# Performance work log

Measured on AMD Instinct MI355X. Metric: run time of the kernel, lower is better.

The kernel has to match this reference:

```python
import jax, jax.numpy as jnp
import numpy as np

B, T, E, C, I_E, O = 4, 2048, 8, 512, 512, 4096


def setup_inputs() -> dict:
    key = jax.random.key(0)
    k1, k2, k3, k4 = jax.random.split(key, 4)
    x = jax.random.normal(k1, (B, E, C, I_E), dtype=jnp.float32)
    combine_array = jax.random.uniform(k2, (B, T, E, C), dtype=jnp.float32)
    W = jax.random.normal(k3, (E, O, I_E), dtype=jnp.float32) * (1.0 / np.sqrt(I_E))
    b = jax.random.normal(k4, (O,), dtype=jnp.float32) * 0.02
    return {"x": x, "combine_array": combine_array, "W": W, "b": b}


def reference(x, combine_array, W, b):
    # per-expert grouped GEMM: [B,E,C,I_e] x [E,O,I_e] -> [B,E,C,O]
    expert_outputs = jnp.einsum('beci,eoi->beco', x, W) + b
    # expert-choice combine: [B,E,C,O] x [B,T,E,C] -> [B,T,O]
    combined = jnp.einsum('beco,btec->bto', expert_outputs, combine_array)
    return combined
```

## Files before the change

kernel.cpp:

```cpp
#include <hip/hip_runtime.h>
#include <hip/hip_bf16.h>
#include <cstdint>

constexpr int NB = 4;
constexpr int NT = 2048;
constexpr int NE = 8;
constexpr int NC = 512;
constexpr int NI = 512;
constexpr int NO = 4096;
constexpr int NEC = NE * NC;

typedef __attribute__((ext_vector_type(8))) short short8;
typedef __attribute__((ext_vector_type(8))) unsigned short ushort8;
typedef __attribute__((ext_vector_type(4))) float f32x4;

__device__ __forceinline__ unsigned short f2bf(float f) {
  unsigned int u = __builtin_bit_cast(unsigned int, f);
  u += 0x7FFFu + ((u >> 16) & 1u);
  return (unsigned short)(u >> 16);
}

__device__ __forceinline__ ushort8 cvt8(float4 a, float4 b) {
  ushort8 v;
  v[0] = f2bf(a.x); v[1] = f2bf(a.y); v[2] = f2bf(a.z); v[3] = f2bf(a.w);
  v[4] = f2bf(b.x); v[5] = f2bf(b.y); v[6] = f2bf(b.z); v[7] = f2bf(b.w);
  return v;
}

__device__ __forceinline__ int lds_byte(int row, int kbyte) {
  return (row * 64 + kbyte) ^ ((row & 6) << 3);
}

__device__ __forceinline__ void gload_lds16(const void* g, void* lds) {
  __builtin_amdgcn_global_load_lds(
      (const __attribute__((address_space(1))) unsigned int*)g,
      (__attribute__((address_space(3))) unsigned int*)lds, 16, 0, 0);
}

__global__ __launch_bounds__(256) void k_cvt(
    const float* __restrict__ src, unsigned short* __restrict__ dst, int n8) {
  int i = blockIdx.x * blockDim.x + threadIdx.x;
  const int stride = gridDim.x * blockDim.x;
  for (; i < n8; i += stride) {
    const float4* s = (const float4*)(src + (size_t)i * 8);
    float4 a = s[0], b = s[1];
    *(ushort8*)(dst + (size_t)i * 8) = cvt8(a, b);
  }
}

template <int NKT>
__device__ __forceinline__ void gemm8_core(
    const unsigned short* __restrict__ Ag,
    const unsigned short* __restrict__ Bg,
    const int ldk, unsigned short* lds, f32x4 (&acc)[8][4]) {
  const int tid = threadIdx.x, lane = tid & 63, wv = tid >> 6;
  const int wr = wv >> 2, wc = wv & 3;
  const int g16 = lane >> 4;
  const int fr  = lane & 15;
  const int pc  = (g16 ^ ((fr >> 1) & 3)) << 4;

  const int scg = (lane & 3) ^ ((lane >> 3) & 3);
  const size_t srow0 = (size_t)(wv * 16 + (lane >> 2)) * ldk + scg * 8;
  const size_t srowstep = (size_t)128 * ldk;
  const int sdst0 = wv * 512;

#define ASLOT(D, KH) ((D) * 16384 + (KH) * 8192)
#define BSLOT(D, KH) (32768 + (D) * 16384 + (KH) * 8192)
#define STG(PTR, SLOT, KT, KH)                                                \
  {                                                                           \
    const unsigned short* _g = (PTR) + srow0 + (size_t)(KT) * 64 + (KH) * 32; \
    gload_lds16(_g, lds + (SLOT) + sdst0);                                    \
    gload_lds16(_g + srowstep, lds + (SLOT) + 4096 + sdst0);                  \
  }
#define RD8(SLOT, R) \
  (*(const short8*)((const char*)lds + (SLOT) * 2 + (R) * 64 + pc))

  short8 afA[4], afB[4], bfA[4], bfB[4];

#define LDA4(SET, D, KH, MH)                                        \
  _Pragma("unroll") for (int m = 0; m < 4; ++m) {                   \
    SET[m] = RD8(ASLOT(D, KH), wr * 128 + (MH) * 64 + m * 16 + fr); \
  }
#define LDB4(SET, D, KH)                                            \
  _Pragma("unroll") for (int n = 0; n < 4; ++n) {                   \
    SET[n] = RD8(BSLOT(D, KH), wc * 64 + n * 16 + fr);              \
  }
#define MFMAQ(ASET, BSET, MH)                                        \
  __builtin_amdgcn_s_setprio(1);                                     \
  _Pragma("unroll") for (int m = 0; m < 4; ++m)                      \
  _Pragma("unroll") for (int n = 0; n < 4; ++n) {                    \
    acc[(MH) * 4 + m][n] = __builtin_amdgcn_mfma_f32_16x16x32_bf16(  \
        ASET[m], BSET[n], acc[(MH) * 4 + m][n], 0, 0, 0);            \
  }                                                                  \
  __builtin_amdgcn_s_setprio(0);
#define LG4()                                          \
  asm volatile("s_waitcnt lgkmcnt(4)" ::: "memory");   \
  __builtin_amdgcn_sched_barrier(0)
#define LG8()                                          \
  asm volatile("s_waitcnt lgkmcnt(8)" ::: "memory");   \
  __builtin_amdgcn_sched_barrier(0)
#define VM6() asm volatile("s_waitcnt vmcnt(6)" ::: "memory")
#define BAR() __builtin_amdgcn_s_barrier()

  STG(Ag, ASLOT(0, 0), 0, 0); STG(Bg, BSLOT(0, 0), 0, 0);
  STG(Ag, ASLOT(0, 1), 0, 1); STG(Bg, BSLOT(0, 1), 0, 1);
  STG(Ag, ASLOT(1, 0), 1, 0); STG(Bg, BSLOT(1, 0), 1, 0);
  asm volatile("s_waitcnt vmcnt(8)" ::: "memory");
  BAR();
  LDA4(afA, 0, 0, 0); LDB4(bfA, 0, 0);

  for (int it = 0; it < NKT / 2; ++it) {
    const int k1 = (2 * it + 1) & (NKT - 1);
    const int k2 = (2 * it + 2) & (NKT - 1);
    const int k3 = (2 * it + 3) & (NKT - 1);
    STG(Ag, ASLOT(1, 1), k1, 1);
    VM6();
    LDA4(afB, 0, 0, 1);
    LG4();
    MFMAQ(afA, bfA, 0);
    BAR();
    STG(Bg, BSLOT(1, 1), k1, 1);
    LDA4(afA, 0, 1, 0); LDB4(bfB, 0, 1);
    LG8();
    MFMAQ(afB, bfA, 1);
    BAR();
    STG(Ag, ASLOT(0, 0), k2, 0);
    VM6();
    LDA4(afB, 0, 1, 1);
    LG4();
    MFMAQ(afA, bfB, 0);
    BAR();
    STG(Bg, BSLOT(0, 0), k2, 0);
    LDA4(afA, 1, 0, 0); LDB4(bfA, 1, 0);
    LG8();
    MFMAQ(afB, bfB, 1);
    BAR();
    STG(Ag, ASLOT(0, 1), k2, 1);
    VM6();
    LDA4(afB, 1, 0, 1);
    LG4();
    MFMAQ(afA, bfA, 0);
    BAR();
    STG(Bg, BSLOT(0, 1), k2, 1);
    LDA4(afA, 1, 1, 0); LDB4(bfB, 1, 1);
    LG8();
    MFMAQ(afB, bfA, 1);
    BAR();
    STG(Ag, ASLOT(1, 0), k3, 0);
    VM6();
    LDA4(afB, 1, 1, 1);
    LG4();
    MFMAQ(afA, bfB, 0);
    BAR();
    STG(Bg, BSLOT(1, 0), k3, 0);
    LDA4(afA, 0, 0, 0); LDB4(bfA, 0, 0);
    LG8();
    MFMAQ(afB, bfB, 1);
    BAR();
  }
  asm volatile("s_waitcnt vmcnt(0) lgkmcnt(0)" ::: "memory");
#undef ASLOT
#undef BSLOT
#undef STG
#undef RD8
#undef LDA4
#undef LDB4
#undef MFMAQ
#undef LG4
#undef LG8
#undef VM6
#undef BAR
}

__global__ __launch_bounds__(512, 2) void k_gemm1p(
    const unsigned short* __restrict__ Wb, const unsigned short* __restrict__ xb,
    const float* __restrict__ bias, unsigned short* __restrict__ eoT) {
  const int bid = (blockIdx.x & 7) * 128 + (blockIdx.x >> 3);
  const int be = bid >> 5, tile = bid & 31;
  const int b = be >> 3, e = be & 7;
  const int bm = tile >> 1, bn = tile & 1;

  const int tid = threadIdx.x, lane = tid & 63, wv = tid >> 6;
  const int wr = wv >> 2, wc = wv & 3;
  const int g16 = lane >> 4, fr = lane & 15;

  const unsigned short* Ag = Wb + (size_t)e * NO * NI + (size_t)(bm * 256) * NI;
  const unsigned short* Bg = xb + ((size_t)b * NE + e) * NC * NI + (size_t)(bn * 256) * NI;

  __shared__ __align__(16) unsigned short lds[65536];

  f32x4 acc[8][4];
#pragma unroll
  for (int m = 0; m < 8; ++m)
#pragma unroll
    for (int n = 0; n < 4; ++n) acc[m][n] = (f32x4)0.f;

  gemm8_core<NI / 64>(Ag, Bg, NI, lds, acc);

  const int o0 = bm * 256 + wr * 128;
  const int c0 = bn * 256 + wc * 64;
#pragma unroll
  for (int i = 0; i < 8; ++i) {
#pragma unroll
    for (int j = 0; j < 4; ++j) {
      const int o = o0 + (i >> 2) * 64 + (i & 3) * 16 + g16 * 4 + j;
      const float bv = bias[o];
      const size_t base = (((size_t)b * NO + o) * NE + e) * NC + c0;
#pragma unroll
      for (int n = 0; n < 4; ++n)
        eoT[base + n * 16 + fr] = f2bf(acc[i][n][j] + bv);
    }
  }
}

__global__ __launch_bounds__(512, 2) void k_gemm2p(
    const unsigned short* __restrict__ cb, const unsigned short* __restrict__ eoT,
    float* __restrict__ out) {
  const int bid = (blockIdx.x & 7) * 64 + (blockIdx.x >> 3);
  const int b  = bid >> 7;
  const int bm = (bid >> 4) & 7;
  const int bn = bid & 15;

  const int tid = threadIdx.x, lane = tid & 63, wv = tid >> 6;
  const int wr = wv >> 2, wc = wv & 3;
  const int g16 = lane >> 4, fr = lane & 15;

  const unsigned short* Ag = cb  + (size_t)b * NT * NEC + (size_t)(bm * 256) * NEC;
  const unsigned short* Bg = eoT + (size_t)b * NO * NEC + (size_t)(bn * 256) * NEC;

  __shared__ __align__(16) unsigned short lds[65536];

  f32x4 acc[8][4];
#pragma unroll
  for (int m = 0; m < 8; ++m)
#pragma unroll
    for (int n = 0; n < 4; ++n) acc[m][n] = (f32x4)0.f;

  gemm8_core<NEC / 64>(Ag, Bg, NEC, lds, acc);

  const int t0 = bm * 256 + wr * 128;
  const int o0 = bn * 256 + wc * 64;
#pragma unroll
  for (int i = 0; i < 8; ++i) {
#pragma unroll
    for (int j = 0; j < 4; ++j) {
      const int t = t0 + (i >> 2) * 64 + (i & 3) * 16 + g16 * 4 + j;
      float* op = out + ((size_t)b * NT + t) * NO + o0;
#pragma unroll
      for (int n = 0; n < 4; ++n) op[n * 16 + fr] = acc[i][n][j];
    }
  }
}

__global__ __launch_bounds__(256, 2) void k_gemm1(
    const float* __restrict__ x, const float* __restrict__ W,
    const float* __restrict__ bias, unsigned short* __restrict__ eoT) {
  const int tile = blockIdx.x;
  const int e = blockIdx.y, b = blockIdx.z;
  const int bm = tile >> 2, bn = tile & 3;
  const int tid = threadIdx.x, lane = tid & 63, wv = tid >> 6;
  const int wr = wv >> 1, wc = wv & 1;

  const float* Ag = W + (size_t)e * NO * NI + (size_t)(bm * 128) * NI;
  const float* Bg = x + ((size_t)b * NE + e) * NC * NI + (size_t)(bn * 128) * NI;

  __shared__ __align__(16) unsigned short As[128 * 32];
  __shared__ __align__(16) unsigned short Bs[128 * 32];

  f32x4 acc[4][4];
#pragma unroll
  for (int m = 0; m < 4; ++m)
#pragma unroll
    for (int n = 0; n < 4; ++n) acc[m][n] = (f32x4)0.f;

  for (int k0 = 0; k0 < NI; k0 += 32) {
    __syncthreads();
#pragma unroll
    for (int s = 0; s < 2; ++s) {
      const int q = tid + s * 256;
      const int row = q >> 2, kc = (q & 3) * 8;
      const float* ga = Ag + (size_t)row * NI + k0 + kc;
      float4 a0 = *(const float4*)ga;
      float4 a1 = *(const float4*)(ga + 4);
      *(ushort8*)((char*)As + lds_byte(row, kc * 2)) = cvt8(a0, a1);
      const float* gb = Bg + (size_t)row * NI + k0 + kc;
      float4 b0 = *(const float4*)gb;
      float4 b1 = *(const float4*)(gb + 4);
      *(ushort8*)((char*)Bs + lds_byte(row, kc * 2)) = cvt8(b0, b1);
    }
    __syncthreads();

    const int kb = (lane >> 4) * 16;
    short8 af[4], bfv[4];
#pragma unroll
    for (int m = 0; m < 4; ++m) {
      const int r = wr * 64 + m * 16 + (lane & 15);
      af[m] = *(const short8*)((const char*)As + lds_byte(r, kb));
    }
#pragma unroll
    for (int n = 0; n < 4; ++n) {
      const int r = wc * 64 + n * 16 + (lane & 15);
      bfv[n] = *(const short8*)((const char*)Bs + lds_byte(r, kb));
    }
#pragma unroll
    for (int m = 0; m < 4; ++m)
#pragma unroll
      for (int n = 0; n < 4; ++n)
        acc[m][n] = __builtin_amdgcn_mfma_f32_16x16x32_bf16(
            af[m], bfv[n], acc[m][n], 0, 0, 0);
  }

  const int o0 = bm * 128 + wr * 64;
  const int c0 = bn * 128 + wc * 64;
#pragma unroll
  for (int m = 0; m < 4; ++m) {
#pragma unroll
    for (int j = 0; j < 4; ++j) {
      const int o = o0 + m * 16 + (lane >> 4) * 4 + j;
      const float bv = bias[o];
      const size_t base = (((size_t)b * NO + o) * NE + e) * NC + c0;
#pragma unroll
      for (int n = 0; n < 4; ++n)
        eoT[base + n * 16 + (lane & 15)] = f2bf(acc[m][n][j] + bv);
    }
  }
}

__global__ __launch_bounds__(256, 2) void k_gemm2(
    const float* __restrict__ comb, const unsigned short* __restrict__ eoT,
    float* __restrict__ out) {
  const int b = blockIdx.y;
  const int bm = blockIdx.x >> 5;
  const int bn = blockIdx.x & 31;
  const int tid = threadIdx.x, lane = tid & 63, wv = tid >> 6;
  const int wr = wv >> 1, wc = wv & 1;

  const float* Ag = comb + (size_t)b * NT * NEC + (size_t)(bm * 128) * NEC;
  const unsigned short* Bg = eoT + (size_t)b * NO * NEC + (size_t)(bn * 128) * NEC;

  __shared__ __align__(16) unsigned short As[128 * 32];
  __shared__ __align__(16) unsigned short Bs[128 * 32];

  f32x4 acc[4][4];
#pragma unroll
  for (int m = 0; m < 4; ++m)
#pragma unroll
    for (int n = 0; n < 4; ++n) acc[m][n] = (f32x4)0.f;

  for (int k0 = 0; k0 < NEC; k0 += 32) {
    __syncthreads();
#pragma unroll
    for (int s = 0; s < 2; ++s) {
      const int q = tid + s * 256;
      const int row = q >> 2, kc = (q & 3) * 8;
      const float* ga = Ag + (size_t)row * NEC + k0 + kc;
      float4 a0 = *(const float4*)ga;
      float4 a1 = *(const float4*)(ga + 4);
      *(ushort8*)((char*)As + lds_byte(row, kc * 2)) = cvt8(a0, a1);
      ushort8 bv = *(const ushort8*)(Bg + (size_t)row * NEC + k0 + kc);
      *(ushort8*)((char*)Bs + lds_byte(row, kc * 2)) = bv;
    }
    __syncthreads();

    const int kb = (lane >> 4) * 16;
    short8 af[4], bfv[4];
#pragma unroll
    for (int m = 0; m < 4; ++m) {
      const int r = wr * 64 + m * 16 + (lane & 15);
      af[m] = *(const short8*)((const char*)As + lds_byte(r, kb));
    }
#pragma unroll
    for (int n = 0; n < 4; ++n) {
      const int r = wc * 64 + n * 16 + (lane & 15);
      bfv[n] = *(const short8*)((const char*)Bs + lds_byte(r, kb));
    }
#pragma unroll
    for (int m = 0; m < 4; ++m)
#pragma unroll
      for (int n = 0; n < 4; ++n)
        acc[m][n] = __builtin_amdgcn_mfma_f32_16x16x32_bf16(
            af[m], bfv[n], acc[m][n], 0, 0, 0);
  }

  const int t0 = bm * 128 + wr * 64;
  const int o0 = bn * 128 + wc * 64;
#pragma unroll
  for (int m = 0; m < 4; ++m) {
#pragma unroll
    for (int j = 0; j < 4; ++j) {
      const int t = t0 + m * 16 + (lane >> 4) * 4 + j;
      float* op = out + ((size_t)b * NT + t) * NO + o0;
#pragma unroll
      for (int n = 0; n < 4; ++n) op[n * 16 + (lane & 15)] = acc[m][n][j];
    }
  }
}

extern "C" void kernel_launch(void* const* d_in, const int* in_sizes, int n_in,
                              void* d_out, int out_size, void* d_ws, size_t ws_size,
                              hipStream_t stream) {
  const float* x    = (const float*)d_in[0];
  const float* comb = (const float*)d_in[1];
  const float* W    = (const float*)d_in[2];
  const float* bias = (const float*)d_in[3];
  float* out = (float*)d_out;

  const size_t EOT_ELEMS = (size_t)NB * NO * NE * NC;
  const size_t X_ELEMS   = (size_t)NB * NE * NC * NI;
  const size_t W_ELEMS   = (size_t)NE * NO * NI;
  const size_t C_ELEMS   = (size_t)NB * NT * NE * NC;
  const size_t region2_elems = (C_ELEMS > X_ELEMS + W_ELEMS) ? C_ELEMS : (X_ELEMS + W_ELEMS);
  const size_t need = (EOT_ELEMS + region2_elems) * 2;

  unsigned short* eoT = (unsigned short*)d_ws;

  if (ws_size >= need) {
    unsigned short* reg2 = eoT + EOT_ELEMS;
    unsigned short* xb = reg2;
    unsigned short* Wb = reg2 + X_ELEMS;
    unsigned short* cbp = reg2;

    k_cvt<<<2048, 256, 0, stream>>>(x, xb, (int)(X_ELEMS / 8));
    k_cvt<<<2048, 256, 0, stream>>>(W, Wb, (int)(W_ELEMS / 8));
    k_gemm1p<<<1024, 512, 0, stream>>>(Wb, xb, bias, eoT);
    k_cvt<<<2048, 256, 0, stream>>>(comb, cbp, (int)(C_ELEMS / 8));
    k_gemm2p<<<512, 512, 0, stream>>>(cbp, eoT, out);
  } else {
    k_gemm1<<<dim3(128, NE, NB), 256, 0, stream>>>(x, W, bias, eoT);
    k_gemm2<<<dim3(512, NB), 256, 0, stream>>>(comb, eoT, out);
  }
}
```

Before: 396.6 us.

## Reassociate MoE combine: contract combine weights with x before expert projection

Reorders the two contractions so the combine array is first multiplied with the expert inputs per expert (producing a [B,T,E,I] intermediate), followed by one GEMM against transposed expert weights over E*I. The bias is applied afterward as bias times the per-token sum of combine weights, computed during combine conversion. This lowers the first GEMM's work and halves the intermediate size, but adds transposing conversions for x and W and rounds a different intermediate to bf16.

New measurement: 354.4 us. -10.6%, faster.

```diff
diff --git a/kernel.cpp b/kernel.cpp
--- a/kernel.cpp
+++ b/kernel.cpp
@@ -9,6 +9,7 @@
 constexpr int NI = 512;
 constexpr int NO = 4096;
 constexpr int NEC = NE * NC;
+constexpr int NEI = NE * NI;
 
 typedef __attribute__((ext_vector_type(8))) short short8;
 typedef __attribute__((ext_vector_type(8))) unsigned short ushort8;
@@ -37,14 +38,65 @@
       (__attribute__((address_space(3))) unsigned int*)lds, 16, 0, 0);
 }
 
-__global__ __launch_bounds__(256) void k_cvt(
-    const float* __restrict__ src, unsigned short* __restrict__ dst, int n8) {
-  int i = blockIdx.x * blockDim.x + threadIdx.x;
-  const int stride = gridDim.x * blockDim.x;
-  for (; i < n8; i += stride) {
-    const float4* s = (const float4*)(src + (size_t)i * 8);
-    float4 a = s[0], b = s[1];
-    *(ushort8*)(dst + (size_t)i * 8) = cvt8(a, b);
+
+__global__ __launch_bounds__(256) void k_cvt_comb(
+    const float* __restrict__ comb, unsigned short* __restrict__ cbp,
+    float* __restrict__ S) {
+  const int row = blockIdx.x;
+  const float* src = comb + (size_t)row * NEC;
+  unsigned short* dst = cbp + (size_t)row * NEC;
+  const int tid = threadIdx.x;
+  float sum = 0.f;
+#pragma unroll
+  for (int it = 0; it < 2; ++it) {
+    const int i8 = tid + it * 256;
+    const float4* s = (const float4*)(src + i8 * 8);
+    float4 a = s[0], b4 = s[1];
+    *(ushort8*)(dst + i8 * 8) = cvt8(a, b4);
+    sum += a.x + a.y + a.z + a.w + b4.x + b4.y + b4.z + b4.w;
+  }
+  for (int off = 32; off > 0; off >>= 1) sum += __shfl_down(sum, off);
+  __shared__ float ws4[4];
+  if ((tid & 63) == 0) ws4[tid >> 6] = sum;
+  __syncthreads();
+  if (tid == 0) S[row] = ws4[0] + ws4[1] + ws4[2] + ws4[3];
+}
+
+__global__ __launch_bounds__(256) void k_cvtT_x(
+    const float* __restrict__ x, unsigned short* __restrict__ xT) {
+  const int be = blockIdx.x >> 6;
+  const int tile = blockIdx.x & 63;
+  const int c0 = (tile >> 3) * 64, i0 = (tile & 7) * 64;
+  const float* src = x + (size_t)be * NC * NI;
+  unsigned short* dst = xT + (size_t)be * NI * NC;
+  __shared__ unsigned short tl[64][65];
+  const int lr = threadIdx.x >> 6, lc = threadIdx.x & 63;
+#pragma unroll
+  for (int s = 0; s < 16; ++s) {
+    const int c = s * 4 + lr;
+    tl[c][lc] = f2bf(src[(size_t)(c0 + c) * NI + i0 + lc]);
+  }
+  __syncthreads();
+#pragma unroll
+  for (int s = 0; s < 16; ++s) {
+    const int i = s * 4 + lr;
+    dst[(size_t)(i0 + i) * NC + c0 + lc] = tl[lc][i];
+  }
+}
+
+__global__ __launch_bounds__(256) void k_cvtT_W(
+    const float* __restrict__ W, unsigned short* __restrict__ Wt) {
+  const size_t n8 = (size_t)NE * NO * NI / 8;
+  size_t idx = (size_t)blockIdx.x * 256 + threadIdx.x;
+  const size_t stride = (size_t)gridDim.x * 256;
+  for (; idx < n8; idx += stride) {
+    const int i8 = (int)(idx & (NI / 8 - 1));
+    const size_t eo = idx >> 6;
+    const int e = (int)(eo >> 12);
+    const int o = (int)(eo & 4095);
+    const float4* s = (const float4*)(W + eo * NI + i8 * 8);
+    float4 a = s[0], b4 = s[1];
+    *(ushort8*)(Wt + ((size_t)o * NE + e) * NI + i8 * 8) = cvt8(a, b4);
   }
 }
 
@@ -52,7 +104,7 @@
 __device__ __forceinline__ void gemm8_core(
     const unsigned short* __restrict__ Ag,
     const unsigned short* __restrict__ Bg,
-    const int ldk, unsigned short* lds, f32x4 (&acc)[8][4]) {
+    const int ldkA, const int ldkB, unsigned short* lds, f32x4 (&acc)[8][4]) {
   const int tid = threadIdx.x, lane = tid & 63, wv = tid >> 6;
   const int wr = wv >> 2, wc = wv & 3;
   const int g16 = lane >> 4;
@@ -60,17 +112,19 @@
   const int pc  = (g16 ^ ((fr >> 1) & 3)) << 4;
 
   const int scg = (lane & 3) ^ ((lane >> 3) & 3);
-  const size_t srow0 = (size_t)(wv * 16 + (lane >> 2)) * ldk + scg * 8;
-  const size_t srowstep = (size_t)128 * ldk;
+  const size_t srow0A = (size_t)(wv * 16 + (lane >> 2)) * ldkA + scg * 8;
+  const size_t srow0B = (size_t)(wv * 16 + (lane >> 2)) * ldkB + scg * 8;
+  const size_t srstA = (size_t)128 * ldkA;
+  const size_t srstB = (size_t)128 * ldkB;
   const int sdst0 = wv * 512;
 
 #define ASLOT(D, KH) ((D) * 16384 + (KH) * 8192)
 #define BSLOT(D, KH) (32768 + (D) * 16384 + (KH) * 8192)
-#define STG(PTR, SLOT, KT, KH)                                                \
-  {                                                                           \
-    const unsigned short* _g = (PTR) + srow0 + (size_t)(KT) * 64 + (KH) * 32; \
-    gload_lds16(_g, lds + (SLOT) + sdst0);                                    \
-    gload_lds16(_g + srowstep, lds + (SLOT) + 4096 + sdst0);                  \
+#define STG(PTR, SR0, SRST, SLOT, KT, KH)                                  \
+  {                                                                        \
+    const unsigned short* _g = (PTR) + (SR0) + (size_t)(KT) * 64 + (KH) * 32; \
+    gload_lds16(_g, lds + (SLOT) + sdst0);                                 \
+    gload_lds16(_g + (SRST), lds + (SLOT) + 4096 + sdst0);                 \
   }
 #define RD8(SLOT, R) \
   (*(const short8*)((const char*)lds + (SLOT) * 2 + (R) * 64 + pc))
@@ -102,9 +156,12 @@
 #define VM6() asm volatile("s_waitcnt vmcnt(6)" ::: "memory")
 #define BAR() __builtin_amdgcn_s_barrier()
 
-  STG(Ag, ASLOT(0, 0), 0, 0); STG(Bg, BSLOT(0, 0), 0, 0);
-  STG(Ag, ASLOT(0, 1), 0, 1); STG(Bg, BSLOT(0, 1), 0, 1);
-  STG(Ag, ASLOT(1, 0), 1, 0); STG(Bg, BSLOT(1, 0), 1, 0);
+  STG(Ag, srow0A, srstA, ASLOT(0, 0), 0, 0);
+  STG(Bg, srow0B, srstB, BSLOT(0, 0), 0, 0);
+  STG(Ag, srow0A, srstA, ASLOT(0, 1), 0, 1);
+  STG(Bg, srow0B, srstB, BSLOT(0, 1), 0, 1);
+  STG(Ag, srow0A, srstA, ASLOT(1, 0), 1, 0);
+  STG(Bg, srow0B, srstB, BSLOT(1, 0), 1, 0);
   asm volatile("s_waitcnt vmcnt(8)" ::: "memory");
   BAR();
   LDA4(afA, 0, 0, 0); LDB4(bfA, 0, 0);
@@ -113,46 +170,46 @@
     const int k1 = (2 * it + 1) & (NKT - 1);
     const int k2 = (2 * it + 2) & (NKT - 1);
     const int k3 = (2 * it + 3) & (NKT - 1);
-    STG(Ag, ASLOT(1, 1), k1, 1);
+    STG(Ag, srow0A, srstA, ASLOT(1, 1), k1, 1);
     VM6();
     LDA4(afB, 0, 0, 1);
     LG4();
     MFMAQ(afA, bfA, 0);
     BAR();
-    STG(Bg, BSLOT(1, 1), k1, 1);
+    STG(Bg, srow0B, srstB, BSLOT(1, 1), k1, 1);
     LDA4(afA, 0, 1, 0); LDB4(bfB, 0, 1);
     LG8();
     MFMAQ(afB, bfA, 1);
     BAR();
-    STG(Ag, ASLOT(0, 0), k2, 0);
+    STG(Ag, srow0A, srstA, ASLOT(0, 0), k2, 0);
     VM6();
     LDA4(afB, 0, 1, 1);
     LG4();
     MFMAQ(afA, bfB, 0);
     BAR();
-    STG(Bg, BSLOT(0, 0), k2, 0);
+    STG(Bg, srow0B, srstB, BSLOT(0, 0), k2, 0);
     LDA4(afA, 1, 0, 0); LDB4(bfA, 1, 0);
     LG8();
     MFMAQ(afB, bfB, 1);
     BAR();
-    STG(Ag, ASLOT(0, 1), k2, 1);
+    STG(Ag, srow0A, srstA, ASLOT(0, 1), k2, 1);
     VM6();
     LDA4(afB, 1, 0, 1);
     LG4();
     MFMAQ(afA, bfA, 0);
     BAR();
-    STG(Bg, BSLOT(0, 1), k2, 1);
+    STG(Bg, srow0B, srstB, BSLOT(0, 1), k2, 1);
     LDA4(afA, 1, 1, 0); LDB4(bfB, 1, 1);
     LG8();
     MFMAQ(afB, bfA, 1);
     BAR();
-    STG(Ag, ASLOT(1, 0), k3, 0);
+    STG(Ag, srow0A, srstA, ASLOT(1, 0), k3, 0);
     VM6();
     LDA4(afB, 1, 1, 1);
     LG4();
     MFMAQ(afA, bfB, 0);
     BAR();
-    STG(Bg, BSLOT(1, 0), k3, 0);
+    STG(Bg, srow0B, srstB, BSLOT(1, 0), k3, 0);
     LDA4(afA, 0, 0, 0); LDB4(bfA, 0, 0);
     LG8();
     MFMAQ(afB, bfB, 1);
@@ -172,11 +229,11 @@
 #undef BAR
 }
 
-__global__ __launch_bounds__(512, 2) void k_gemm1p(
-    const unsigned short* __restrict__ Wb, const unsigned short* __restrict__ xb,
-    const float* __restrict__ bias, unsigned short* __restrict__ eoT) {
-  const int bid = (blockIdx.x & 7) * 128 + (blockIdx.x >> 3);
-  const int be = bid >> 5, tile = bid & 31;
+__global__ __launch_bounds__(512, 2) void k_gemm1q(
+    const unsigned short* __restrict__ cbp, const unsigned short* __restrict__ xT,
+    unsigned short* __restrict__ Y) {
+  const int bid = (blockIdx.x & 7) * 64 + (blockIdx.x >> 3);
+  const int be = bid >> 4, tile = bid & 15;
   const int b = be >> 3, e = be & 7;
   const int bm = tile >> 1, bn = tile & 1;
 
@@ -184,8 +241,10 @@
   const int wr = wv >> 2, wc = wv & 3;
   const int g16 = lane >> 4, fr = lane & 15;
 
-  const unsigned short* Ag = Wb + (size_t)e * NO * NI + (size_t)(bm * 256) * NI;
-  const unsigned short* Bg = xb + ((size_t)b * NE + e) * NC * NI + (size_t)(bn * 256) * NI;
+  const unsigned short* Ag =
+      cbp + (size_t)b * NT * NEC + (size_t)(bm * 256) * NEC + e * NC;
+  const unsigned short* Bg =
+      xT + (size_t)be * NI * NC + (size_t)(bn * 256) * NC;
 
   __shared__ __align__(16) unsigned short lds[65536];
 
@@ -195,26 +254,25 @@
 #pragma unroll
     for (int n = 0; n < 4; ++n) acc[m][n] = (f32x4)0.f;
 
-  gemm8_core<NI / 64>(Ag, Bg, NI, lds, acc);
-
-  const int o0 = bm * 256 + wr * 128;
-  const int c0 = bn * 256 + wc * 64;
-#pragma unroll
-  for (int i = 0; i < 8; ++i) {
+  gemm8_core<NC / 64>(Ag, Bg, NEC, NC, lds, acc);
+
+  const int t0 = bm * 256 + wr * 128;
+  const int i0c = bn * 256 + wc * 64;
+#pragma unroll
+  for (int ii = 0; ii < 8; ++ii) {
 #pragma unroll
     for (int j = 0; j < 4; ++j) {
-      const int o = o0 + (i >> 2) * 64 + (i & 3) * 16 + g16 * 4 + j;
-      const float bv = bias[o];
-      const size_t base = (((size_t)b * NO + o) * NE + e) * NC + c0;
-#pragma unroll
-      for (int n = 0; n < 4; ++n)
-        eoT[base + n * 16 + fr] = f2bf(acc[i][n][j] + bv);
-    }
-  }
-}
-
-__global__ __launch_bounds__(512, 2) void k_gemm2p(
-    const unsigned short* __restrict__ cb, const unsigned short* __restrict__ eoT,
+      const int t = t0 + (ii >> 2) * 64 + (ii & 3) * 16 + g16 * 4 + j;
+      unsigned short* yp = Y + ((size_t)b * NT + t) * NEI + e * NI + i0c;
+#pragma unroll
+      for (int n = 0; n < 4; ++n) yp[n * 16 + fr] = f2bf(acc[ii][n][j]);
+    }
+  }
+}
+
+__global__ __launch_bounds__(512, 2) void k_gemm2q(
+    const unsigned short* __restrict__ Y, const unsigned short* __restrict__ Wt,
+    const float* __restrict__ bias, const float* __restrict__ S,
     float* __restrict__ out) {
   const int bid = (blockIdx.x & 7) * 64 + (blockIdx.x >> 3);
   const int b  = bid >> 7;
@@ -225,8 +283,8 @@
   const int wr = wv >> 2, wc = wv & 3;
   const int g16 = lane >> 4, fr = lane & 15;
 
-  const unsigned short* Ag = cb  + (size_t)b * NT * NEC + (size_t)(bm * 256) * NEC;
-  const unsigned short* Bg = eoT + (size_t)b * NO * NEC + (size_t)(bn * 256) * NEC;
+  const unsigned short* Ag = Y + (size_t)b * NT * NEI + (size_t)(bm * 256) * NEI;
+  const unsigned short* Bg = Wt + (size_t)(bn * 256) * NEI;
 
   __shared__ __align__(16) unsigned short lds[65536];
 
@@ -236,18 +294,22 @@
 #pragma unroll
     for (int n = 0; n < 4; ++n) acc[m][n] = (f32x4)0.f;
 
-  gemm8_core<NEC / 64>(Ag, Bg, NEC, lds, acc);
+  gemm8_core<NEI / 64>(Ag, Bg, NEI, NEI, lds, acc);
 
   const int t0 = bm * 256 + wr * 128;
   const int o0 = bn * 256 + wc * 64;
-#pragma unroll
-  for (int i = 0; i < 8; ++i) {
+  float bv[4];
+#pragma unroll
+  for (int n = 0; n < 4; ++n) bv[n] = bias[o0 + n * 16 + fr];
+#pragma unroll
+  for (int ii = 0; ii < 8; ++ii) {
 #pragma unroll
     for (int j = 0; j < 4; ++j) {
-      const int t = t0 + (i >> 2) * 64 + (i & 3) * 16 + g16 * 4 + j;
+      const int t = t0 + (ii >> 2) * 64 + (ii & 3) * 16 + g16 * 4 + j;
+      const float sv = S[b * NT + t];
       float* op = out + ((size_t)b * NT + t) * NO + o0;
 #pragma unroll
-      for (int n = 0; n < 4; ++n) op[n * 16 + fr] = acc[i][n][j];
+      for (int n = 0; n < 4; ++n) op[n * 16 + fr] = acc[ii][n][j] + bv[n] * sv;
     }
   }
 }
@@ -317,11 +379,11 @@
 #pragma unroll
     for (int j = 0; j < 4; ++j) {
       const int o = o0 + m * 16 + (lane >> 4) * 4 + j;
-      const float bv = bias[o];
+      const float bvv = bias[o];
       const size_t base = (((size_t)b * NO + o) * NE + e) * NC + c0;
 #pragma unroll
       for (int n = 0; n < 4; ++n)
-        eoT[base + n * 16 + (lane & 15)] = f2bf(acc[m][n][j] + bv);
+        eoT[base + n * 16 + (lane & 15)] = f2bf(acc[m][n][j] + bvv);
     }
   }
 }
@@ -357,8 +419,8 @@
       float4 a0 = *(const float4*)ga;
       float4 a1 = *(const float4*)(ga + 4);
       *(ushort8*)((char*)As + lds_byte(row, kc * 2)) = cvt8(a0, a1);
-      ushort8 bv = *(const ushort8*)(Bg + (size_t)row * NEC + k0 + kc);
-      *(ushort8*)((char*)Bs + lds_byte(row, kc * 2)) = bv;
+      ushort8 bvv = *(const ushort8*)(Bg + (size_t)row * NEC + k0 + kc);
+      *(ushort8*)((char*)Bs + lds_byte(row, kc * 2)) = bvv;
     }
     __syncthreads();
 
@@ -405,27 +467,27 @@
   const float* bias = (const float*)d_in[3];
   float* out = (float*)d_out;
 
-  const size_t EOT_ELEMS = (size_t)NB * NO * NE * NC;
-  const size_t X_ELEMS   = (size_t)NB * NE * NC * NI;
-  const size_t W_ELEMS   = (size_t)NE * NO * NI;
-  const size_t C_ELEMS   = (size_t)NB * NT * NE * NC;
-  const size_t region2_elems = (C_ELEMS > X_ELEMS + W_ELEMS) ? C_ELEMS : (X_ELEMS + W_ELEMS);
-  const size_t need = (EOT_ELEMS + region2_elems) * 2;
-
-  unsigned short* eoT = (unsigned short*)d_ws;
+  const size_t Y_ELEMS  = (size_t)NB * NT * NEI;
+  const size_t C_ELEMS  = (size_t)NB * NT * NEC;
+  const size_t XT_ELEMS = (size_t)NB * NE * NI * NC;
+  const size_t WT_ELEMS = (size_t)NO * NE * NI;
+  const size_t need =
+      (Y_ELEMS + C_ELEMS + XT_ELEMS + WT_ELEMS) * 2 + (size_t)NB * NT * 4;
 
   if (ws_size >= need) {
-    unsigned short* reg2 = eoT + EOT_ELEMS;
-    unsigned short* xb = reg2;
-    unsigned short* Wb = reg2 + X_ELEMS;
-    unsigned short* cbp = reg2;
-
-    k_cvt<<<2048, 256, 0, stream>>>(x, xb, (int)(X_ELEMS / 8));
-    k_cvt<<<2048, 256, 0, stream>>>(W, Wb, (int)(W_ELEMS / 8));
-    k_gemm1p<<<1024, 512, 0, stream>>>(Wb, xb, bias, eoT);
-    k_cvt<<<2048, 256, 0, stream>>>(comb, cbp, (int)(C_ELEMS / 8));
-    k_gemm2p<<<512, 512, 0, stream>>>(cbp, eoT, out);
+    unsigned short* Yp  = (unsigned short*)d_ws;
+    unsigned short* cbp = Yp + Y_ELEMS;
+    unsigned short* xT  = cbp + C_ELEMS;
+    unsigned short* Wt  = xT + XT_ELEMS;
+    float* S = (float*)(Wt + WT_ELEMS);
+
+    k_cvtT_x<<<2048, 256, 0, stream>>>(x, xT);
+    k_cvt_comb<<<NB * NT, 256, 0, stream>>>(comb, cbp, S);
+    k_gemm1q<<<512, 512, 0, stream>>>(cbp, xT, Yp);
+    k_cvtT_W<<<2048, 256, 0, stream>>>(W, Wt);
+    k_gemm2q<<<512, 512, 0, stream>>>(Yp, Wt, bias, S, out);
   } else {
+    unsigned short* eoT = (unsigned short*)d_ws;
     k_gemm1<<<dim3(128, NE, NB), 256, 0, stream>>>(x, W, bias, eoT);
     k_gemm2<<<dim3(512, NB), 256, 0, stream>>>(comb, eoT, out);
   }
```
